# Performance work log

Measured on AMD Instinct MI355X. Metric: run time of the kernel, lower is better.

## Reference

```python
import jax, jax.numpy as jnp
import numpy as np

N, IN_DIM, OUT_DIM, HEADS = 3072, 512, 64, 8
EDGE_PROB = 0.01
NEG_SLOPE = 0.2


def setup_inputs() -> dict:
    key = jax.random.key(0)
    k1, k2, k3, k4, k5 = jax.random.split(key, 5)
    x = jax.random.normal(k1, (N, IN_DIM), dtype=jnp.float32)
    # sparse-ish dense adjacency mask with self-loops
    adj = (jax.random.uniform(k2, (N, N)) < EDGE_PROB).astype(jnp.float32)
    adj = jnp.maximum(adj, jnp.eye(N, dtype=jnp.float32))
    W = jax.random.normal(k3, (HEADS, IN_DIM, OUT_DIM), dtype=jnp.float32) * 0.1
    a_src = jax.random.normal(k4, (HEADS, OUT_DIM), dtype=jnp.float32) * 0.1
    a_dst = jax.random.normal(k5, (HEADS, OUT_DIM), dtype=jnp.float32) * 0.1
    return {"x": x, "adj": adj, "W": W, "a_src": a_src, "a_dst": a_dst}


def reference(x, adj, W, a_src, a_dst):
    # per-head linear projection: [H, N, OUT]
    h = jnp.einsum("ni,hio->hno", x, W)
    # attention logits e_ij = LeakyReLU(a_src . h_i + a_dst . h_j)
    f_src = jnp.einsum("hno,ho->hn", h, a_src)  # [H, N]
    f_dst = jnp.einsum("hno,ho->hn", h, a_dst)  # [H, N]
    e = f_src[:, :, None] + f_dst[:, None, :]   # [H, N, N]
    e = jax.nn.leaky_relu(e, negative_slope=NEG_SLOPE)
    # mask non-edges, row-softmax over neighbors
    e = jnp.where(adj[None] > 0, e, jnp.float32(-1e9))
    att = jax.nn.softmax(e, axis=-1)             # [H, N, N]
    # aggregate neighbor features per head
    out = jnp.einsum("hij,hjo->hio", att, h)     # [H, N, OUT]
    # concat heads along feature dim -> [N, H*OUT]
    return out.transpose(1, 0, 2).reshape(N, HEADS * OUT_DIM)
```

## Files before the change

kernel.cpp:

```cpp
#include <hip/hip_runtime.h>

#define N_NODES 3072
#define IN_DIM 512
#define OUT_DIM 64
#define HEADS 8
#define NEG_SLOPE 0.2f
#define MAX_E 256

#define MT 32
#define KT 32
#define AS_LD 40
#define BS_LD 40

typedef __attribute__((ext_vector_type(8))) short bf16x8;
typedef __attribute__((ext_vector_type(4))) float f32x4;

__device__ inline unsigned short f2bf(float f) {
    union { float f; unsigned u; } v; v.f = f;
    unsigned r = (v.u + 0x7FFF + ((v.u >> 16) & 1)) >> 16;
    return (unsigned short)r;
}

__device__ inline float waveAllMax(float v) {
#pragma unroll
    for (int o = 32; o; o >>= 1) v = fmaxf(v, __shfl_xor(v, o, 64));
    return v;
}
__device__ inline float waveAllSum(float v) {
#pragma unroll
    for (int o = 32; o; o >>= 1) v += __shfl_xor(v, o, 64);
    return v;
}

__global__ __launch_bounds__(256) void gat_proj(
    const float* __restrict__ x, const float* __restrict__ W,
    const float* __restrict__ a_src, const float* __restrict__ a_dst,
    float* __restrict__ hbuf, float* __restrict__ fsrc, float* __restrict__ fdst) {
    __shared__ unsigned short As[MT][AS_LD];
    __shared__ unsigned short Bs[OUT_DIM][BS_LD];
    __shared__ float hs[MT][OUT_DIM + 1];

    const int t = threadIdx.x;
    const int head = blockIdx.y;
    const int m0 = blockIdx.x * MT;
    const int lane = t & 63;
    const int w = t >> 6;
    const int rt = w & 1;
    const int ct0 = (w >> 1) * 2;

    const float* Wh = W + (size_t)head * IN_DIM * OUT_DIM;

    f32x4 acc0 = {0.f, 0.f, 0.f, 0.f};
    f32x4 acc1 = {0.f, 0.f, 0.f, 0.f};

    const int arow = t >> 3;
    const int acol = (t & 7) * 4;
    const int bk   = t >> 3;
    const int bn0  = (t & 7) * 8;

    for (int ks = 0; ks < IN_DIM; ks += KT) {
        __syncthreads();
        float4 av = *(const float4*)(x + (size_t)(m0 + arow) * IN_DIM + ks + acol);
        As[arow][acol + 0] = f2bf(av.x);
        As[arow][acol + 1] = f2bf(av.y);
        As[arow][acol + 2] = f2bf(av.z);
        As[arow][acol + 3] = f2bf(av.w);
        const float* wp = Wh + (size_t)(ks + bk) * OUT_DIM + bn0;
        float4 b0 = *(const float4*)(wp);
        float4 b1 = *(const float4*)(wp + 4);
        Bs[bn0 + 0][bk] = f2bf(b0.x);
        Bs[bn0 + 1][bk] = f2bf(b0.y);
        Bs[bn0 + 2][bk] = f2bf(b0.z);
        Bs[bn0 + 3][bk] = f2bf(b0.w);
        Bs[bn0 + 4][bk] = f2bf(b1.x);
        Bs[bn0 + 5][bk] = f2bf(b1.y);
        Bs[bn0 + 6][bk] = f2bf(b1.z);
        Bs[bn0 + 7][bk] = f2bf(b1.w);
        __syncthreads();

        const int q = lane >> 4;
        bf16x8 afrag  = *(const bf16x8*)&As[(lane & 15) + rt * 16][q * 8];
        bf16x8 bfrag0 = *(const bf16x8*)&Bs[(lane & 15) + ct0 * 16][q * 8];
        bf16x8 bfrag1 = *(const bf16x8*)&Bs[(lane & 15) + (ct0 + 1) * 16][q * 8];
        acc0 = __builtin_amdgcn_mfma_f32_16x16x32_bf16(afrag, bfrag0, acc0, 0, 0, 0);
        acc1 = __builtin_amdgcn_mfma_f32_16x16x32_bf16(afrag, bfrag1, acc1, 0, 0, 0);
    }

    {
        const int col0 = ct0 * 16 + (lane & 15);
        const int row_b = rt * 16 + (lane >> 4) * 4;
#pragma unroll
        for (int i = 0; i < 4; ++i) {
            const int r = row_b + i;
            hs[r][col0] = acc0[i];
            hs[r][col0 + 16] = acc1[i];
            float* gp = hbuf + ((size_t)head * N_NODES + m0 + r) * OUT_DIM;
            gp[col0] = acc0[i];
            gp[col0 + 16] = acc1[i];
        }
    }
    __syncthreads();

    {
        const float* av = (t < 128 ? a_src : a_dst) + head * OUT_DIM;
        const int tt = t & 127;
        const int row = tt >> 2, part = tt & 3;
        float s = 0.f;
#pragma unroll
        for (int n = 0; n < 16; ++n) s += hs[row][part * 16 + n] * av[part * 16 + n];
        s += __shfl_xor(s, 1, 64);
        s += __shfl_xor(s, 2, 64);
        if (part == 0) {
            float* dst = (t < 128 ? fsrc : fdst);
            dst[head * N_NODES + m0 + row] = s;
        }
    }
}

__global__ __launch_bounds__(256) void gat_agg(
    const float* __restrict__ adj, const float* __restrict__ hbuf,
    const float* __restrict__ fsrc, const float* __restrict__ fdst,
    float* __restrict__ out) {
    __shared__ int s_idx[MAX_E];
    __shared__ float s_p[4][MAX_E];
    __shared__ int s_cnt;

    const int i = blockIdx.x;
    const int t = threadIdx.x;
    if (t == 0) s_cnt = 0;
    __syncthreads();

    const float4* arow4 = (const float4*)(adj + (size_t)i * N_NODES);
#pragma unroll
    for (int it = 0; it < 3; ++it) {
        const int jj = t + it * 256;
        float4 v = arow4[jj];
        const int j = jj * 4;
        if (v.x > 0.f) { int s = atomicAdd(&s_cnt, 1); if (s < MAX_E) s_idx[s] = j; }
        if (v.y > 0.f) { int s = atomicAdd(&s_cnt, 1); if (s < MAX_E) s_idx[s] = j + 1; }
        if (v.z > 0.f) { int s = atomicAdd(&s_cnt, 1); if (s < MAX_E) s_idx[s] = j + 2; }
        if (v.w > 0.f) { int s = atomicAdd(&s_cnt, 1); if (s < MAX_E) s_idx[s] = j + 3; }
    }
    __syncthreads();
    const int E = min(s_cnt, MAX_E);
    const int w = t >> 6;
    const int lane = t & 63;

    for (int head = w; head < HEADS; head += 4) {
        const float fi = fsrc[head * N_NODES + i];

        float m = -1e30f;
        for (int k = lane; k < E; k += 64) {
            float e = fi + fdst[head * N_NODES + s_idx[k]];
            e = e > 0.f ? e : NEG_SLOPE * e;
            s_p[w][k] = e;
            m = fmaxf(m, e);
        }
        m = waveAllMax(m);

        float sum = 0.f;
        for (int k = lane; k < E; k += 64) {
            float p = __expf(s_p[w][k] - m);
            s_p[w][k] = p;
            sum += p;
        }
        sum = waveAllSum(sum);
        const float inv = 1.f / sum;

        float acc = 0.f;
#pragma unroll 4
        for (int k = 0; k < E; ++k) {
            acc = fmaf(s_p[w][k],
                       hbuf[((size_t)head * N_NODES + s_idx[k]) * OUT_DIM + lane],
                       acc);
        }
        out[(size_t)i * (HEADS * OUT_DIM) + head * OUT_DIM + lane] = acc * inv;
    }
}

extern "C" void kernel_launch(void* const* d_in, const int* in_sizes, int n_in,
                              void* d_out, int out_size, void* d_ws, size_t ws_size,
                              hipStream_t stream) {
    const float* x     = (const float*)d_in[0];
    const float* adj   = (const float*)d_in[1];
    const float* W     = (const float*)d_in[2];
    const float* a_src = (const float*)d_in[3];
    const float* a_dst = (const float*)d_in[4];
    float* out = (float*)d_out;

    float* hbuf = (float*)d_ws;
    float* fsrc = hbuf + (size_t)HEADS * N_NODES * OUT_DIM;
    float* fdst = fsrc + HEADS * N_NODES;

    gat_proj<<<dim3(N_NODES / MT, HEADS), 256, 0, stream>>>(x, W, a_src, a_dst,
                                                            hbuf, fsrc, fdst);
    gat_agg<<<N_NODES, 256, 0, stream>>>(adj, hbuf, fsrc, fdst, out);
}
```

Baseline: 129.0 us.

## Pre-pack x and W into MFMA fragment layout and interleave heads in aggregation

Adds a prep kernel that converts x and W to bf16 once and stores them directly in the per-lane MFMA fragment order. The projection kernel then loads fragments straight from global memory with no shared-memory staging or per-K-tile barriers. The aggregation kernel now handles two heads per wave at once and stores each neighbour index alongside its weight, so two independent gather streams can overlap. MAX_E is lowered to 128, which assumes no node has more than 128 neighbours, and the extra launch adds a pass over x and W.

```diff
diff --git a/kernel.cpp b/kernel.cpp
--- a/kernel.cpp
+++ b/kernel.cpp
@@ -5,15 +5,15 @@
 #define OUT_DIM 64
 #define HEADS 8
 #define NEG_SLOPE 0.2f
-#define MAX_E 256
-
-#define MT 32
-#define KT 32
-#define AS_LD 40
-#define BS_LD 40
+#define MAX_E 128
 
 typedef __attribute__((ext_vector_type(8))) short bf16x8;
 typedef __attribute__((ext_vector_type(4))) float f32x4;
+
+#define XFRAG_TILES (N_NODES / 16)
+#define KTILES (IN_DIM / 32)
+#define XFRAG_THREADS (XFRAG_TILES * KTILES * 64)
+#define WFRAG_THREADS (HEADS * KTILES * 4 * 64)
 
 __device__ inline unsigned short f2bf(float f) {
     union { float f; unsigned u; } v; v.f = f;
@@ -32,72 +32,77 @@
     return v;
 }
 
+__global__ __launch_bounds__(256) void gat_prep(
+    const float* __restrict__ x, const float* __restrict__ W,
+    short* __restrict__ xfrag, short* __restrict__ wfrag) {
+    int tid = blockIdx.x * 256 + threadIdx.x;
+    if (tid < XFRAG_THREADS) {
+        int lane = tid & 63;
+        int kt = (tid >> 6) & (KTILES - 1);
+        int rt = tid >> 10;
+        int m = rt * 16 + (lane & 15);
+        int k0 = kt * 32 + (lane >> 4) * 8;
+        const float4* xp = (const float4*)(x + (size_t)m * IN_DIM + k0);
+        float4 v0 = xp[0], v1 = xp[1];
+        bf16x8 r;
+        r[0] = (short)f2bf(v0.x); r[1] = (short)f2bf(v0.y);
+        r[2] = (short)f2bf(v0.z); r[3] = (short)f2bf(v0.w);
+        r[4] = (short)f2bf(v1.x); r[5] = (short)f2bf(v1.y);
+        r[6] = (short)f2bf(v1.z); r[7] = (short)f2bf(v1.w);
+        ((bf16x8*)xfrag)[tid] = r;
+    } else {
+        int t2 = tid - XFRAG_THREADS;
+        if (t2 >= WFRAG_THREADS) return;
+        int lane = t2 & 63;
+        int c = (t2 >> 6) & 3;
+        int kt = (t2 >> 8) & (KTILES - 1);
+        int head = t2 >> 12;
+        int n = c * 16 + (lane & 15);
+        int k0 = kt * 32 + (lane >> 4) * 8;
+        const float* wp = W + ((size_t)head * IN_DIM + k0) * OUT_DIM + n;
+        bf16x8 r;
+#pragma unroll
+        for (int j = 0; j < 8; ++j) r[j] = (short)f2bf(wp[(size_t)j * OUT_DIM]);
+        ((bf16x8*)wfrag)[t2] = r;
+    }
+}
+
 __global__ __launch_bounds__(256) void gat_proj(
-    const float* __restrict__ x, const float* __restrict__ W,
+    const short* __restrict__ xfrag, const short* __restrict__ wfrag,
     const float* __restrict__ a_src, const float* __restrict__ a_dst,
     float* __restrict__ hbuf, float* __restrict__ fsrc, float* __restrict__ fdst) {
-    __shared__ unsigned short As[MT][AS_LD];
-    __shared__ unsigned short Bs[OUT_DIM][BS_LD];
-    __shared__ float hs[MT][OUT_DIM + 1];
+    __shared__ float hs[32][OUT_DIM + 1];
 
     const int t = threadIdx.x;
-    const int head = blockIdx.y;
-    const int m0 = blockIdx.x * MT;
     const int lane = t & 63;
     const int w = t >> 6;
-    const int rt = w & 1;
-    const int ct0 = (w >> 1) * 2;
-
-    const float* Wh = W + (size_t)head * IN_DIM * OUT_DIM;
+    const int head = blockIdx.y;
+    const int m0 = blockIdx.x * 32;
+    const int rt0 = blockIdx.x * 2;
+
+    const bf16x8* xa = (const bf16x8*)xfrag + (size_t)rt0 * 16 * 64 + lane;
+    const bf16x8* wb = (const bf16x8*)wfrag + ((size_t)head * KTILES * 4 + w) * 64 + lane;
 
     f32x4 acc0 = {0.f, 0.f, 0.f, 0.f};
     f32x4 acc1 = {0.f, 0.f, 0.f, 0.f};
-
-    const int arow = t >> 3;
-    const int acol = (t & 7) * 4;
-    const int bk   = t >> 3;
-    const int bn0  = (t & 7) * 8;
-
-    for (int ks = 0; ks < IN_DIM; ks += KT) {
-        __syncthreads();
-        float4 av = *(const float4*)(x + (size_t)(m0 + arow) * IN_DIM + ks + acol);
-        As[arow][acol + 0] = f2bf(av.x);
-        As[arow][acol + 1] = f2bf(av.y);
-        As[arow][acol + 2] = f2bf(av.z);
-        As[arow][acol + 3] = f2bf(av.w);
-        const float* wp = Wh + (size_t)(ks + bk) * OUT_DIM + bn0;
-        float4 b0 = *(const float4*)(wp);
-        float4 b1 = *(const float4*)(wp + 4);
-        Bs[bn0 + 0][bk] = f2bf(b0.x);
-        Bs[bn0 + 1][bk] = f2bf(b0.y);
-        Bs[bn0 + 2][bk] = f2bf(b0.z);
-        Bs[bn0 + 3][bk] = f2bf(b0.w);
-        Bs[bn0 + 4][bk] = f2bf(b1.x);
-        Bs[bn0 + 5][bk] = f2bf(b1.y);
-        Bs[bn0 + 6][bk] = f2bf(b1.z);
-        Bs[bn0 + 7][bk] = f2bf(b1.w);
-        __syncthreads();
-
-        const int q = lane >> 4;
-        bf16x8 afrag  = *(const bf16x8*)&As[(lane & 15) + rt * 16][q * 8];
-        bf16x8 bfrag0 = *(const bf16x8*)&Bs[(lane & 15) + ct0 * 16][q * 8];
-        bf16x8 bfrag1 = *(const bf16x8*)&Bs[(lane & 15) + (ct0 + 1) * 16][q * 8];
-        acc0 = __builtin_amdgcn_mfma_f32_16x16x32_bf16(afrag, bfrag0, acc0, 0, 0, 0);
-        acc1 = __builtin_amdgcn_mfma_f32_16x16x32_bf16(afrag, bfrag1, acc1, 0, 0, 0);
-    }
-
-    {
-        const int col0 = ct0 * 16 + (lane & 15);
-        const int row_b = rt * 16 + (lane >> 4) * 4;
-#pragma unroll
-        for (int i = 0; i < 4; ++i) {
-            const int r = row_b + i;
-            hs[r][col0] = acc0[i];
-            hs[r][col0 + 16] = acc1[i];
-            float* gp = hbuf + ((size_t)head * N_NODES + m0 + r) * OUT_DIM;
-            gp[col0] = acc0[i];
-            gp[col0 + 16] = acc1[i];
-        }
+#pragma unroll
+    for (int kt = 0; kt < KTILES; ++kt) {
+        bf16x8 a0 = xa[kt * 64];
+        bf16x8 a1 = xa[(16 + kt) * 64];
+        bf16x8 b  = wb[kt * 4 * 64];
+        acc0 = __builtin_amdgcn_mfma_f32_16x16x32_bf16(a0, b, acc0, 0, 0, 0);
+        acc1 = __builtin_amdgcn_mfma_f32_16x16x32_bf16(a1, b, acc1, 0, 0, 0);
+    }
+
+    const int col = w * 16 + (lane & 15);
+    const int r0 = (lane >> 4) * 4;
+    float* gp = hbuf + ((size_t)head * N_NODES + m0) * OUT_DIM;
+#pragma unroll
+    for (int i2 = 0; i2 < 4; ++i2) {
+        hs[r0 + i2][col] = acc0[i2];
+        hs[r0 + 16 + i2][col] = acc1[i2];
+        gp[(size_t)(r0 + i2) * OUT_DIM + col] = acc0[i2];
+        gp[(size_t)(r0 + 16 + i2) * OUT_DIM + col] = acc1[i2];
     }
     __syncthreads();
 
@@ -122,7 +127,7 @@
     const float* __restrict__ fsrc, const float* __restrict__ fdst,
     float* __restrict__ out) {
     __shared__ int s_idx[MAX_E];
-    __shared__ float s_p[4][MAX_E];
+    __shared__ float s_pe[4][2][2 * MAX_E];
     __shared__ int s_cnt;
 
     const int i = blockIdx.x;
@@ -145,37 +150,43 @@
     const int E = min(s_cnt, MAX_E);
     const int w = t >> 6;
     const int lane = t & 63;
-
-    for (int head = w; head < HEADS; head += 4) {
-        const float fi = fsrc[head * N_NODES + i];
-
-        float m = -1e30f;
-        for (int k = lane; k < E; k += 64) {
-            float e = fi + fdst[head * N_NODES + s_idx[k]];
-            e = e > 0.f ? e : NEG_SLOPE * e;
-            s_p[w][k] = e;
-            m = fmaxf(m, e);
-        }
-        m = waveAllMax(m);
-
-        float sum = 0.f;
-        for (int k = lane; k < E; k += 64) {
-            float p = __expf(s_p[w][k] - m);
-            s_p[w][k] = p;
-            sum += p;
-        }
-        sum = waveAllSum(sum);
-        const float inv = 1.f / sum;
-
-        float acc = 0.f;
-#pragma unroll 4
-        for (int k = 0; k < E; ++k) {
-            acc = fmaf(s_p[w][k],
-                       hbuf[((size_t)head * N_NODES + s_idx[k]) * OUT_DIM + lane],
-                       acc);
-        }
-        out[(size_t)i * (HEADS * OUT_DIM) + head * OUT_DIM + lane] = acc * inv;
-    }
+    const int h0 = w, h1 = w + 4;
+
+    const float fiA = fsrc[h0 * N_NODES + i];
+    const float fiB = fsrc[h1 * N_NODES + i];
+
+    float mA = -1e30f, mB = -1e30f;
+    for (int k = lane; k < E; k += 64) {
+        int j = s_idx[k];
+        float eA = fiA + fdst[h0 * N_NODES + j];
+        float eB = fiB + fdst[h1 * N_NODES + j];
+        eA = eA > 0.f ? eA : NEG_SLOPE * eA;
+        eB = eB > 0.f ? eB : NEG_SLOPE * eB;
+        s_pe[w][0][2 * k] = eA; s_pe[w][0][2 * k + 1] = __int_as_float(j);
+        s_pe[w][1][2 * k] = eB; s_pe[w][1][2 * k + 1] = __int_as_float(j);
+        mA = fmaxf(mA, eA); mB = fmaxf(mB, eB);
+    }
+    mA = waveAllMax(mA); mB = waveAllMax(mB);
+
+    float sA = 0.f, sB = 0.f;
+    for (int k = lane; k < E; k += 64) {
+        float pA = __expf(s_pe[w][0][2 * k] - mA); s_pe[w][0][2 * k] = pA; sA += pA;
+        float pB = __expf(s_pe[w][1][2 * k] - mB); s_pe[w][1][2 * k] = pB; sB += pB;
+    }
+    sA = waveAllSum(sA); sB = waveAllSum(sB);
+    const float invA = 1.f / sA, invB = 1.f / sB;
+
+    float accA = 0.f, accB = 0.f;
+#pragma unroll 8
+    for (int k = 0; k < E; ++k) {
+        float2 a = *(const float2*)&s_pe[w][0][2 * k];
+        float2 b = *(const float2*)&s_pe[w][1][2 * k];
+        int ja = __float_as_int(a.y), jb = __float_as_int(b.y);
+        accA = fmaf(a.x, hbuf[((size_t)h0 * N_NODES + ja) * OUT_DIM + lane], accA);
+        accB = fmaf(b.x, hbuf[((size_t)h1 * N_NODES + jb) * OUT_DIM + lane], accB);
+    }
+    out[(size_t)i * (HEADS * OUT_DIM) + h0 * OUT_DIM + lane] = accA * invA;
+    out[(size_t)i * (HEADS * OUT_DIM) + h1 * OUT_DIM + lane] = accB * invB;
 }
 
 extern "C" void kernel_launch(void* const* d_in, const int* in_sizes, int n_in,
@@ -191,8 +202,12 @@
     float* hbuf = (float*)d_ws;
     float* fsrc = hbuf + (size_t)HEADS * N_NODES * OUT_DIM;
     float* fdst = fsrc + HEADS * N_NODES;
-
-    gat_proj<<<dim3(N_NODES / MT, HEADS), 256, 0, stream>>>(x, W, a_src, a_dst,
-                                                            hbuf, fsrc, fdst);
+    short* xfrag = (short*)(fdst + HEADS * N_NODES);
+    short* wfrag = xfrag + (size_t)XFRAG_TILES * KTILES * 64 * 8;
+
+    gat_prep<<<(XFRAG_THREADS + WFRAG_THREADS) / 256, 256, 0, stream>>>(
+        x, W, xfrag, wfrag);
+    gat_proj<<<dim3(N_NODES / 32, HEADS), 256, 0, stream>>>(
+        xfrag, wfrag, a_src, a_dst, hbuf, fsrc, fdst);
     gat_agg<<<N_NODES, 256, 0, stream>>>(adj, hbuf, fsrc, fdst, out);
 }
```

After: 114.9 us. 10.9% less time.
